# Kernel optimization log

Hardware: AMD Instinct MI355X
Metric: run time of the kernel (lower is better)

## Reference

```python
import jax, jax.numpy as jnp
import numpy as np

DIM = 16
BOND = 4
RANK = 512
N = 50000
E = 400000
F_IN = 16
EDGE_VARIABLE = 2


def setup_inputs() -> dict:
    key = jax.random.key(0)
    ks = iter(jax.random.split(key, 48))
    g = lambda shape, s=0.1: jax.random.normal(next(ks), shape, jnp.float32) * s
    inp = {
        "x": jax.random.normal(next(ks), (N, F_IN), jnp.float32),
        "node_type": jax.random.randint(next(ks), (N,), 0, 3),
        "edge_index": jax.random.randint(next(ks), (2, E), 0, N),
        "edge_attr": jax.random.uniform(next(ks), (E, BOND), dtype=jnp.float32),
        # lin0
        "W_lin0": g((F_IN, DIM)), "b_lin0": jnp.zeros((DIM,), jnp.float32),
        # NNConv: root weight + edge-conditioned weight MLP (4 -> 32 -> dim*dim)
        "W_root": g((DIM, DIM)), "b_conv": jnp.zeros((DIM,), jnp.float32),
        "W_e1": g((BOND, 32)), "b_e1": jnp.zeros((32,), jnp.float32),
        "W_e2": g((32, DIM * DIM)), "b_e2": jnp.zeros((DIM * DIM,), jnp.float32),
        # GRU (torch gate order r,z,n), weights stored torch-style [3*dim, dim]
        "W_ih": g((3 * DIM, DIM)), "b_ih": jnp.zeros((3 * DIM,), jnp.float32),
        "W_hh": g((3 * DIM, DIM)), "b_hh": jnp.zeros((3 * DIM,), jnp.float32),
        # projections
        "W_lin1": g((DIM, BOND)), "b_lin1": jnp.zeros((BOND,), jnp.float32),
        "W_up": g((BOND, DIM)), "b_up": jnp.zeros((DIM,), jnp.float32),
        "W_down": g((DIM, BOND)), "b_down": jnp.zeros((BOND,), jnp.float32),
        # FGNet low-rank factor modules (rank 512)
        "U_B": g((DIM, RANK)), "V_B": g((RANK, DIM)),
        "U_C": g((DIM, RANK)), "V_C": g((RANK, DIM)),
        "U_A": g((BOND, RANK)), "V_A": g((RANK, BOND)),
        # fusion weights
        "w_node": g((1, DIM)), "W_lin": g((DIM, DIM)), "b_lin": jnp.zeros((DIM,), jnp.float32),
        "w_edge": g((1, BOND)), "W_line": g((BOND, BOND)), "b_line": jnp.zeros((BOND,), jnp.float32),
    }
    return inp


def _forward(x, edge_attr, W_lin0, b_lin0, W_root, b_conv, W_e1, b_e1, W_e2, b_e2,
             W_ih, b_ih, W_hh, b_hh, W_lin1, b_lin1, W_up, b_up, W_down, b_down,
             U_B, V_B, U_C, V_C, U_A, V_A, w_node, W_lin, b_lin, w_edge, W_line, b_line,
             node_type, edge_index):
    src, dst = edge_index[0], edge_index[1]

    def nnconv(out):
        # per-edge weight matrices from edge features (edge-conditioned conv)
        he = jax.nn.relu(edge_attr @ W_e1 + b_e1)
        We = (he @ W_e2 + b_e2).reshape(E, DIM, DIM)          # [E, dim, dim]
        m = jnp.einsum('ed,edk->ek', out[src], We)             # gather-multiply
        agg = jax.ops.segment_sum(m, dst, num_segments=N)      # scatter-add
        deg = jax.ops.segment_sum(jnp.ones((E,), out.dtype), dst, num_segments=N)
        agg = agg / jnp.clip(deg, 1.0)[:, None]                # mean aggregation
        return out @ W_root + b_conv + agg

    def gru(inp, h):
        gi = inp @ W_ih.T + b_ih
        gh = h @ W_hh.T + b_hh
        i_r, i_z, i_n = jnp.split(gi, 3, axis=-1)
        h_r, h_z, h_n = jnp.split(gh, 3, axis=-1)
        r = jax.nn.sigmoid(i_r + h_r)
        z = jax.nn.sigmoid(i_z + h_z)
        n = jnp.tanh(i_n + r * h_n)
        return (1.0 - z) * n + z * h

    out = jax.nn.relu(x @ W_lin0 + b_lin0)                     # [N, dim]
    h = out
    for _ in range(3):
        m = jax.nn.relu(nnconv(out))
        h = gru(m, h)
        out = h

    out_edges = jax.nn.relu(out @ W_lin1 + b_lin1)             # [N, bond]

    # one outer message-passing round (k in range(1))
    ev_mask = (node_type == EDGE_VARIABLE)[:, None]
    out_edges_up = out_edges @ W_up + b_up                     # [N, dim]
    out_combine = jnp.where(ev_mask, out_edges_up, out)        # masked replace

    # factor-B message (low-rank FGNet) -> node-dim message + down-projected edge msg
    msg_B = jax.nn.relu((out_combine @ U_B) @ V_B)             # [N, dim]
    msg_to_edge_B = msg_B @ W_down + b_down                    # [N, bond]

    # factor-C message (low-rank FGNet)
    msg_C = jax.nn.relu((out_combine @ U_C) @ V_C)             # [N, dim]

    # factor-A / valence message on edge-type beliefs
    msg_to_edge_A = jax.nn.relu((out_edges @ U_A) @ V_A)       # [N, bond]

    all_msg = msg_B + msg_C                                    # sum over stacked msgs
    combine_edge_msg = msg_to_edge_A * msg_to_edge_B

    out = out + jax.nn.relu((w_node * all_msg) @ W_lin + b_lin)
    out_edges = out_edges + jax.nn.relu((w_edge * combine_edge_msg) @ W_line + b_line)

    return jax.nn.log_softmax(out_edges, axis=-1)              # [N, bond]


def reference(x, node_type, edge_index, edge_attr, W_lin0, b_lin0, W_root, b_conv,
              W_e1, b_e1, W_e2, b_e2, W_ih, b_ih, W_hh, b_hh, W_lin1, b_lin1,
              W_up, b_up, W_down, b_down, U_B, V_B, U_C, V_C, U_A, V_A,
              w_node, W_lin, b_lin, w_edge, W_line, b_line):
    return _forward(x, edge_attr, W_lin0, b_lin0, W_root, b_conv, W_e1, b_e1, W_e2, b_e2,
                    W_ih, b_ih, W_hh, b_hh, W_lin1, b_lin1, W_up, b_up, W_down, b_down,
                    U_B, V_B, U_C, V_C, U_A, V_A, w_node, W_lin, b_lin, w_edge, W_line, b_line,
                    node_type, edge_index)
```

## Files before the change

kernel.cpp:

```cpp
#include <hip/hip_runtime.h>
#include <hip/hip_bf16.h>
#include <math.h>

#define N_NODES 50000
#define N_EDGES 400000
#define DIM 16
#define BOND 4
#define NCHUNK 25000
#define EDGE_GRID 784
#define E_BLOCKS 1563
#define PRE_BASE (E_BLOCKS - 68)
#define SCAN_TILE 1024
#define SCAN_BLOCKS 49

typedef __attribute__((ext_vector_type(8))) short short8;
typedef __attribute__((ext_vector_type(4))) float f32x4;

__device__ __forceinline__ float bf16_to_f32(unsigned short v) {
  return __uint_as_float(((unsigned int)v) << 16);
}

__global__ __launch_bounds__(256) void setup_kernel(
    const float* __restrict__ x, const float* __restrict__ W_lin0,
    const float* __restrict__ b_lin0, const float* __restrict__ ea,
    const float* __restrict__ We1, const float* __restrict__ be1,
    const int* __restrict__ ei, const float* __restrict__ U_B,
    const float* __restrict__ V_B, const float* __restrict__ U_A,
    const float* __restrict__ V_A, float* __restrict__ out,
    unsigned int* __restrict__ he_buf, int* __restrict__ degI,
    float* __restrict__ M_B, float* __restrict__ M_A) {
  __shared__ float sW0[256];
  __shared__ float sb0[16];
  __shared__ float sW1[128];
  __shared__ float sb1[32];
  int t = threadIdx.x;
  sW0[t] = W_lin0[t];
  if (t < 16) sb0[t] = b_lin0[t];
  if (t < 128) sW1[t] = We1[t];
  if (t < 32) sb1[t] = be1[t];
  __syncthreads();

  int gid = blockIdx.x * 256 + t;

  if (gid < N_NODES) {
    float xr[16];
#pragma unroll
    for (int d = 0; d < 16; ++d) xr[d] = x[gid * 16 + d];
#pragma unroll
    for (int k = 0; k < 16; ++k) {
      float acc = sb0[k];
#pragma unroll
      for (int d = 0; d < 16; ++d) acc += xr[d] * sW0[d * 16 + k];
      out[gid * 16 + k] = fmaxf(acc, 0.f);
    }
  }

  if (gid < N_EDGES) {
    float4 v = ((const float4*)ea)[gid];
    float h[32];
#pragma unroll
    for (int k = 0; k < 32; ++k) {
      float a = sb1[k] + v.x * sW1[k] + v.y * sW1[32 + k] + v.z * sW1[64 + k] +
                v.w * sW1[96 + k];
      h[k] = fmaxf(a, 0.f);
    }
    unsigned int u[16];
#pragma unroll
    for (int p = 0; p < 2; ++p)
#pragma unroll
      for (int tt = 0; tt < 8; ++tt) {
        float2 pr;
        pr.x = h[4 * tt + p];
        pr.y = h[4 * tt + 2 + p];
        __hip_bfloat162 b = __float22bfloat162_rn(pr);
        u[p * 8 + tt] = *(unsigned int*)&b;
      }
    uint4* dst = (uint4*)(he_buf + (size_t)gid * 16);
#pragma unroll
    for (int qq = 0; qq < 4; ++qq)
      dst[qq] =
          make_uint4(u[4 * qq], u[4 * qq + 1], u[4 * qq + 2], u[4 * qq + 3]);
    atomicAdd(&degI[ei[N_EDGES + gid]], 1);
  }

  if (blockIdx.x >= PRE_BASE) {
    int w = (blockIdx.x - PRE_BASE) * 4 + (t >> 6);
    int lane = t & 63;
    float partial = 0.f;
    if (w < 256) {
      int i = w >> 4, j = w & 15;
#pragma unroll
      for (int r8 = 0; r8 < 8; ++r8) {
        int r = lane + 64 * r8;
        partial += U_B[i * 512 + r] * V_B[r * 16 + j];
      }
    } else if (w < 272) {
      int a = (w - 256) >> 2, b = (w - 256) & 3;
#pragma unroll
      for (int r8 = 0; r8 < 8; ++r8) {
        int r = lane + 64 * r8;
        partial += U_A[a * 512 + r] * V_A[r * 4 + b];
      }
    }
#pragma unroll
    for (int off = 32; off > 0; off >>= 1)
      partial += __shfl_down(partial, off);
    if (lane == 0) {
      if (w < 256) M_B[w] = partial;
      else if (w < 272) M_A[w - 256] = partial;
    }
  }
}

__global__ __launch_bounds__(256) void scan_kernel(
    const int* __restrict__ degI, int* ticket, int* st,
    int* __restrict__ row_off, int* __restrict__ cur) {
  __shared__ int sdata[256];
  __shared__ int s_tile;
  __shared__ int s_base;
  int t = threadIdx.x;
  if (t == 0) s_tile = atomicAdd(ticket, 1);
  __syncthreads();
  int tile = s_tile;
  int n0 = tile * SCAN_TILE + t * 4;

  int d0 = (n0 + 0 < N_NODES) ? degI[n0 + 0] : 0;
  int d1 = (n0 + 1 < N_NODES) ? degI[n0 + 1] : 0;
  int d2 = (n0 + 2 < N_NODES) ? degI[n0 + 2] : 0;
  int d3 = (n0 + 3 < N_NODES) ? degI[n0 + 3] : 0;
  int tsum = d0 + d1 + d2 + d3;
  sdata[t] = tsum;
  __syncthreads();
  for (int off = 1; off < 256; off <<= 1) {
    int v = (t >= off) ? sdata[t - off] : 0;
    __syncthreads();
    sdata[t] += v;
    __syncthreads();
  }
  int excl = sdata[t] - tsum;
  int agg = sdata[255];

  if (t == 0) {
    if (tile == 0) {
      atomicExch(&st[0], (agg << 2) | 2);
      s_base = 0;
    } else {
      atomicExch(&st[tile], (agg << 2) | 1);
      int run = 0, idx = tile - 1;
      while (true) {
        int w = atomicAdd(&st[idx], 0);
        int stt = w & 3;
        if (stt == 2) { run += (w >> 2); break; }
        if (stt == 1) { run += (w >> 2); --idx; }
      }
      atomicExch(&st[tile], ((run + agg) << 2) | 2);
      s_base = run;
    }
  }
  __syncthreads();

  int pre = s_base + excl;
  if (n0 + 0 < N_NODES) { row_off[n0 + 0] = pre; cur[n0 + 0] = pre; }
  pre += d0;
  if (n0 + 1 < N_NODES) { row_off[n0 + 1] = pre; cur[n0 + 1] = pre; }
  pre += d1;
  if (n0 + 2 < N_NODES) { row_off[n0 + 2] = pre; cur[n0 + 2] = pre; }
  pre += d2;
  if (n0 + 3 < N_NODES) { row_off[n0 + 3] = pre; cur[n0 + 3] = pre; }
  if (tile == SCAN_BLOCKS - 1 && t == 0) row_off[N_NODES] = N_EDGES;
}

__global__ __launch_bounds__(256) void slot_kernel(const int* __restrict__ ei,
                                                   int* __restrict__ cur,
                                                   int* __restrict__ slot) {
  int e = blockIdx.x * 256 + threadIdx.x;
  if (e < N_EDGES) slot[e] = atomicAdd(&cur[ei[N_EDGES + e]], 1);
}

__global__ __launch_bounds__(256) void edge_msg_mfma_kernel(
    const int* __restrict__ ei, const unsigned int* __restrict__ he_buf,
    const float* __restrict__ We2, const float* __restrict__ be2,
    const float* __restrict__ out, const int* __restrict__ slot,
    unsigned short* __restrict__ m_bufh) {
  const int lane = threadIdx.x & 63;
  const int q = lane >> 4, n = lane & 15;
  const int p = q >> 1, dbase = (q & 1) * 8;

  short8 bfrag[17];
#pragma unroll
  for (int s = 0; s < 16; ++s) {
    int h = 2 * s + p;
    union { short8 v; __hip_bfloat162 b2[4]; } bf;
#pragma unroll
    for (int jj = 0; jj < 4; ++jj) {
      float2 w;
      w.x = We2[h * 256 + (dbase + 2 * jj) * 16 + n];
      w.y = We2[h * 256 + (dbase + 2 * jj + 1) * 16 + n];
      bf.b2[jj] = __float22bfloat162_rn(w);
    }
    bfrag[s] = bf.v;
  }
  {
    union { short8 v; __hip_bfloat162 b2[4]; } bf;
#pragma unroll
    for (int jj = 0; jj < 4; ++jj) {
      float2 w;
      if (q < 2) {
        w.x = be2[(dbase + 2 * jj) * 16 + n];
        w.y = be2[(dbase + 2 * jj + 1) * 16 + n];
      } else {
        w.x = 0.f; w.y = 0.f;
      }
      bf.b2[jj] = __float22bfloat162_rn(w);
    }
    bfrag[16] = bf.v;
  }

  int wave = blockIdx.x * 4 + (threadIdx.x >> 6);
  const int nw = EDGE_GRID * 4;
  for (int c = wave; c < NCHUNK; c += nw) {
    int e = c * 16 + n;
    int src = ei[e];
    const uint4* hp = (const uint4*)(he_buf + (size_t)e * 16 + p * 8);
    uint4 h0 = hp[0], h1 = hp[1];
    unsigned int heu[8] = {h0.x, h0.y, h0.z, h0.w, h1.x, h1.y, h1.z, h1.w};
    const float4* op = (const float4*)(out + src * 16 + dbase);
    float4 o0 = op[0], o1 = op[1];
    float o[8] = {o0.x, o0.y, o0.z, o0.w, o1.x, o1.y, o1.z, o1.w};

    f32x4 acc = {0.f, 0.f, 0.f, 0.f};
#pragma unroll
    for (int s = 0; s < 16; ++s) {
      unsigned int hw = heu[s >> 1];
      float he_s = __uint_as_float((s & 1) ? (hw & 0xffff0000u) : (hw << 16));
      union { short8 v; __hip_bfloat162 b2[4]; } af;
#pragma unroll
      for (int jj = 0; jj < 4; ++jj) {
        float2 pr;
        pr.x = he_s * o[2 * jj];
        pr.y = he_s * o[2 * jj + 1];
        af.b2[jj] = __float22bfloat162_rn(pr);
      }
      acc = __builtin_amdgcn_mfma_f32_16x16x32_bf16(af.v, bfrag[s], acc, 0, 0, 0);
    }
    {
      union { short8 v; __hip_bfloat162 b2[4]; } af;
#pragma unroll
      for (int jj = 0; jj < 4; ++jj) {
        float2 pr;
        if (q < 2) { pr.x = o[2 * jj]; pr.y = o[2 * jj + 1]; }
        else { pr.x = 0.f; pr.y = 0.f; }
        af.b2[jj] = __float22bfloat162_rn(pr);
      }
      acc = __builtin_amdgcn_mfma_f32_16x16x32_bf16(af.v, bfrag[16], acc, 0, 0, 0);
    }

    int4 sl4 = *(const int4*)(slot + c * 16 + q * 4);
    __hip_bfloat16 b0 = __float2bfloat16(acc[0]);
    __hip_bfloat16 b1 = __float2bfloat16(acc[1]);
    __hip_bfloat16 b2 = __float2bfloat16(acc[2]);
    __hip_bfloat16 b3 = __float2bfloat16(acc[3]);
    m_bufh[(size_t)sl4.x * 16 + n] = *(unsigned short*)&b0;
    m_bufh[(size_t)sl4.y * 16 + n] = *(unsigned short*)&b1;
    m_bufh[(size_t)sl4.z * 16 + n] = *(unsigned short*)&b2;
    m_bufh[(size_t)sl4.w * 16 + n] = *(unsigned short*)&b3;
  }
}

__global__ __launch_bounds__(256) void gather_gru_kernel(
    const int* __restrict__ row_off, const unsigned short* __restrict__ m_bufh,
    const float* __restrict__ Wroot, const float* __restrict__ bconv,
    const float* __restrict__ Wih, const float* __restrict__ bih,
    const float* __restrict__ Whh, const float* __restrict__ bhh,
    float* __restrict__ out, int do_final, const int* __restrict__ node_type,
    const float* __restrict__ Wlin1, const float* __restrict__ blin1,
    const float* __restrict__ Wup, const float* __restrict__ bup,
    const float* __restrict__ Wdown, const float* __restrict__ bdown,
    const float* __restrict__ M_B, const float* __restrict__ M_A,
    const float* __restrict__ wedge, const float* __restrict__ Wline,
    const float* __restrict__ bline, float* __restrict__ res) {
  __shared__ float sWr[256];
  __shared__ float sWihT[768];
  __shared__ float sWhhT[768];
  __shared__ float sb[112];
  int t = threadIdx.x;
  int kk = t >> 4, dd = t & 15;
  sWr[t] = Wroot[t];
#pragma unroll
  for (int g = 0; g < 3; ++g) {
    sWihT[g * 256 + dd * 16 + kk] = Wih[g * 256 + t];
    sWhhT[g * 256 + dd * 16 + kk] = Whh[g * 256 + t];
  }
  if (t < 16) sb[t] = bconv[t];
  else if (t < 64) sb[t] = bih[t - 16];
  else if (t < 112) sb[t] = bhh[t - 64];
  __syncthreads();

  int n = blockIdx.x * 16 + (t >> 4);
  int k = t & 15;
  int s0 = row_off[n], s1 = row_off[n + 1];

  float aggk = 0.f;
  for (int j = s0; j < s1; ++j) aggk += bf16_to_f32(m_bufh[(size_t)j * 16 + k]);
  float sc = 1.f / fmaxf((float)(s1 - s0), 1.f);

  float hk = out[n * 16 + k];

  float mk = sb[k] + aggk * sc;
#pragma unroll
  for (int d = 0; d < 16; ++d) mk += __shfl(hk, d, 16) * sWr[d * 16 + k];
  mk = fmaxf(mk, 0.f);

  float gir = sb[16 + k], giz = sb[32 + k], gin = sb[48 + k];
  float ghr = sb[64 + k], ghz = sb[80 + k], ghn = sb[96 + k];
#pragma unroll
  for (int d = 0; d < 16; ++d) {
    float md = __shfl(mk, d, 16);
    float hd = __shfl(hk, d, 16);
    gir += md * sWihT[d * 16 + k];
    giz += md * sWihT[256 + d * 16 + k];
    gin += md * sWihT[512 + d * 16 + k];
    ghr += hd * sWhhT[d * 16 + k];
    ghz += hd * sWhhT[256 + d * 16 + k];
    ghn += hd * sWhhT[512 + d * 16 + k];
  }
  float r = 1.f / (1.f + __expf(-(gir + ghr)));
  float z = 1.f / (1.f + __expf(-(giz + ghz)));
  float xn = gin + r * ghn;
  float ng = 1.f - 2.f / (__expf(2.f * xn) + 1.f);
  float hnew = (1.f - z) * ng + z * hk;

  if (!do_final) {
    out[n * 16 + k] = hnew;
    return;
  }

  float p0 = hnew * Wlin1[k * 4 + 0];
  float p1 = hnew * Wlin1[k * 4 + 1];
  float p2 = hnew * Wlin1[k * 4 + 2];
  float p3 = hnew * Wlin1[k * 4 + 3];
#pragma unroll
  for (int msk = 1; msk < 16; msk <<= 1) {
    p0 += __shfl_xor(p0, msk, 16);
    p1 += __shfl_xor(p1, msk, 16);
    p2 += __shfl_xor(p2, msk, 16);
    p3 += __shfl_xor(p3, msk, 16);
  }
  float oe0 = fmaxf(p0 + blin1[0], 0.f);
  float oe1 = fmaxf(p1 + blin1[1], 0.f);
  float oe2 = fmaxf(p2 + blin1[2], 0.f);
  float oe3 = fmaxf(p3 + blin1[3], 0.f);

  bool ev = (node_type[n] == 2);
  float ock = ev ? (bup[k] + oe0 * Wup[k] + oe1 * Wup[16 + k] +
                    oe2 * Wup[32 + k] + oe3 * Wup[48 + k])
                 : hnew;

  float msgBk = 0.f;
#pragma unroll
  for (int d = 0; d < 16; ++d) msgBk += __shfl(ock, d, 16) * M_B[d * 16 + k];
  msgBk = fmaxf(msgBk, 0.f);

  float q0 = msgBk * Wdown[k * 4 + 0];
  float q1 = msgBk * Wdown[k * 4 + 1];
  float q2 = msgBk * Wdown[k * 4 + 2];
  float q3 = msgBk * Wdown[k * 4 + 3];
#pragma unroll
  for (int msk = 1; msk < 16; msk <<= 1) {
    q0 += __shfl_xor(q0, msk, 16);
    q1 += __shfl_xor(q1, msk, 16);
    q2 += __shfl_xor(q2, msk, 16);
    q3 += __shfl_xor(q3, msk, 16);
  }
  float mtb0 = q0 + bdown[0], mtb1 = q1 + bdown[1];
  float mtb2 = q2 + bdown[2], mtb3 = q3 + bdown[3];

  float mta0 = fmaxf(oe0 * M_A[0] + oe1 * M_A[4] + oe2 * M_A[8] + oe3 * M_A[12], 0.f);
  float mta1 = fmaxf(oe0 * M_A[1] + oe1 * M_A[5] + oe2 * M_A[9] + oe3 * M_A[13], 0.f);
  float mta2 = fmaxf(oe0 * M_A[2] + oe1 * M_A[6] + oe2 * M_A[10] + oe3 * M_A[14], 0.f);
  float mta3 = fmaxf(oe0 * M_A[3] + oe1 * M_A[7] + oe2 * M_A[11] + oe3 * M_A[15], 0.f);

  float c0 = wedge[0] * (mta0 * mtb0);
  float c1 = wedge[1] * (mta1 * mtb1);
  float c2 = wedge[2] * (mta2 * mtb2);
  float c3 = wedge[3] * (mta3 * mtb3);

  float f0 = oe0 + fmaxf(bline[0] + c0 * Wline[0] + c1 * Wline[4] +
                         c2 * Wline[8] + c3 * Wline[12], 0.f);
  float f1 = oe1 + fmaxf(bline[1] + c0 * Wline[1] + c1 * Wline[5] +
                         c2 * Wline[9] + c3 * Wline[13], 0.f);
  float f2 = oe2 + fmaxf(bline[2] + c0 * Wline[2] + c1 * Wline[6] +
                         c2 * Wline[10] + c3 * Wline[14], 0.f);
  float f3 = oe3 + fmaxf(bline[3] + c0 * Wline[3] + c1 * Wline[7] +
                         c2 * Wline[11] + c3 * Wline[15], 0.f);

  float mx = fmaxf(fmaxf(f0, f1), fmaxf(f2, f3));
  float se = __expf(f0 - mx) + __expf(f1 - mx) + __expf(f2 - mx) +
             __expf(f3 - mx);
  float lse = mx + __logf(se);
  if (k < 4) {
    float v = (k == 0) ? f0 : (k == 1) ? f1 : (k == 2) ? f2 : f3;
    res[n * 4 + k] = v - lse;
  }
}

extern "C" void kernel_launch(void* const* d_in, const int* in_sizes, int n_in,
                              void* d_out, int out_size, void* d_ws,
                              size_t ws_size, hipStream_t stream) {
  const float* x       = (const float*)d_in[0];
  const int* node_type = (const int*)d_in[1];
  const int* ei        = (const int*)d_in[2];
  const float* ea      = (const float*)d_in[3];
  const float* W_lin0  = (const float*)d_in[4];
  const float* b_lin0  = (const float*)d_in[5];
  const float* W_root  = (const float*)d_in[6];
  const float* b_conv  = (const float*)d_in[7];
  const float* W_e1    = (const float*)d_in[8];
  const float* b_e1    = (const float*)d_in[9];
  const float* W_e2    = (const float*)d_in[10];
  const float* b_e2    = (const float*)d_in[11];
  const float* W_ih    = (const float*)d_in[12];
  const float* b_ih    = (const float*)d_in[13];
  const float* W_hh    = (const float*)d_in[14];
  const float* b_hh    = (const float*)d_in[15];
  const float* W_lin1  = (const float*)d_in[16];
  const float* b_lin1  = (const float*)d_in[17];
  const float* W_up    = (const float*)d_in[18];
  const float* b_up    = (const float*)d_in[19];
  const float* W_down  = (const float*)d_in[20];
  const float* b_down  = (const float*)d_in[21];
  const float* U_B     = (const float*)d_in[22];
  const float* V_B     = (const float*)d_in[23];
  const float* U_A     = (const float*)d_in[26];
  const float* V_A     = (const float*)d_in[27];
  const float* w_edge  = (const float*)d_in[31];
  const float* W_line  = (const float*)d_in[32];
  const float* b_line  = (const float*)d_in[33];

  float* ws    = (float*)d_ws;
  float* out   = ws;
  unsigned int* he_buf = (unsigned int*)(out + N_NODES * 16);
  unsigned short* m_bufh =
      (unsigned short*)(he_buf + (size_t)N_EDGES * 16);
  float* M_B   = (float*)(m_bufh + (size_t)N_EDGES * 16);
  float* M_A   = M_B + 256;
  int* degI    = (int*)(M_A + 16);
  int* ticket  = degI + N_NODES;
  int* st      = ticket + 1;
  int* row_off = st + 63;
  int* cur     = row_off + N_NODES + 1;
  int* slot    = cur + N_NODES;

  hipMemsetAsync(degI, 0, (N_NODES + 64) * sizeof(int), stream);

  setup_kernel<<<E_BLOCKS, 256, 0, stream>>>(
      x, W_lin0, b_lin0, ea, W_e1, b_e1, ei, U_B, V_B, U_A, V_A, out, he_buf,
      degI, M_B, M_A);
  scan_kernel<<<SCAN_BLOCKS, 256, 0, stream>>>(degI, ticket, st, row_off, cur);
  slot_kernel<<<E_BLOCKS, 256, 0, stream>>>(ei, cur, slot);

  for (int it = 0; it < 3; ++it) {
    edge_msg_mfma_kernel<<<EDGE_GRID, 256, 0, stream>>>(ei, he_buf, W_e2, b_e2,
                                                        out, slot, m_bufh);
    gather_gru_kernel<<<N_NODES / 16, 256, 0, stream>>>(
        row_off, m_bufh, W_root, b_conv, W_ih, b_ih, W_hh, b_hh, out,
        (it == 2) ? 1 : 0, node_type, W_lin1, b_lin1, W_up, b_up, W_down,
        b_down, M_B, M_A, w_edge, W_line, b_line, (float*)d_out);
  }
}
```

Before: 344.8 us.

## Pre-sort edge hidden features and sources by destination to make message writes contiguous

Edge MLP first-layer features and source indices are now computed in the slot kernel and written directly in destination-sorted (CSR) order. The per-iteration edge kernel then reads sorted data and writes messages contiguously, replacing scattered per-slot stores and the slot array. The edge kernel grid is also enlarged to one block per chunk group. In exchange, the he buffer write in setup becomes a scattered write, done once, and source-node gathers in the edge kernel follow sorted order, which is no better localized.

```diff
diff --git a/kernel.cpp b/kernel.cpp
--- a/kernel.cpp
+++ b/kernel.cpp
@@ -4,14 +4,12 @@
 
 #define N_NODES 50000
 #define N_EDGES 400000
-#define DIM 16
-#define BOND 4
 #define NCHUNK 25000
-#define EDGE_GRID 784
 #define E_BLOCKS 1563
 #define PRE_BASE (E_BLOCKS - 68)
 #define SCAN_TILE 1024
 #define SCAN_BLOCKS 49
+#define EDGE_GRID 1563
 
 typedef __attribute__((ext_vector_type(8))) short short8;
 typedef __attribute__((ext_vector_type(4))) float f32x4;
@@ -22,22 +20,16 @@
 
 __global__ __launch_bounds__(256) void setup_kernel(
     const float* __restrict__ x, const float* __restrict__ W_lin0,
-    const float* __restrict__ b_lin0, const float* __restrict__ ea,
-    const float* __restrict__ We1, const float* __restrict__ be1,
-    const int* __restrict__ ei, const float* __restrict__ U_B,
-    const float* __restrict__ V_B, const float* __restrict__ U_A,
-    const float* __restrict__ V_A, float* __restrict__ out,
-    unsigned int* __restrict__ he_buf, int* __restrict__ degI,
-    float* __restrict__ M_B, float* __restrict__ M_A) {
+    const float* __restrict__ b_lin0, const int* __restrict__ ei,
+    const float* __restrict__ U_B, const float* __restrict__ V_B,
+    const float* __restrict__ U_A, const float* __restrict__ V_A,
+    float* __restrict__ out, int* __restrict__ degI, float* __restrict__ M_B,
+    float* __restrict__ M_A) {
   __shared__ float sW0[256];
   __shared__ float sb0[16];
-  __shared__ float sW1[128];
-  __shared__ float sb1[32];
   int t = threadIdx.x;
   sW0[t] = W_lin0[t];
   if (t < 16) sb0[t] = b_lin0[t];
-  if (t < 128) sW1[t] = We1[t];
-  if (t < 32) sb1[t] = be1[t];
   __syncthreads();
 
   int gid = blockIdx.x * 256 + t;
@@ -55,33 +47,7 @@
     }
   }
 
-  if (gid < N_EDGES) {
-    float4 v = ((const float4*)ea)[gid];
-    float h[32];
-#pragma unroll
-    for (int k = 0; k < 32; ++k) {
-      float a = sb1[k] + v.x * sW1[k] + v.y * sW1[32 + k] + v.z * sW1[64 + k] +
-                v.w * sW1[96 + k];
-      h[k] = fmaxf(a, 0.f);
-    }
-    unsigned int u[16];
-#pragma unroll
-    for (int p = 0; p < 2; ++p)
-#pragma unroll
-      for (int tt = 0; tt < 8; ++tt) {
-        float2 pr;
-        pr.x = h[4 * tt + p];
-        pr.y = h[4 * tt + 2 + p];
-        __hip_bfloat162 b = __float22bfloat162_rn(pr);
-        u[p * 8 + tt] = *(unsigned int*)&b;
-      }
-    uint4* dst = (uint4*)(he_buf + (size_t)gid * 16);
-#pragma unroll
-    for (int qq = 0; qq < 4; ++qq)
-      dst[qq] =
-          make_uint4(u[4 * qq], u[4 * qq + 1], u[4 * qq + 2], u[4 * qq + 3]);
-    atomicAdd(&degI[ei[N_EDGES + gid]], 1);
-  }
+  if (gid < N_EDGES) atomicAdd(&degI[ei[N_EDGES + gid]], 1);
 
   if (blockIdx.x >= PRE_BASE) {
     int w = (blockIdx.x - PRE_BASE) * 4 + (t >> 6);
@@ -103,8 +69,7 @@
       }
     }
 #pragma unroll
-    for (int off = 32; off > 0; off >>= 1)
-      partial += __shfl_down(partial, off);
+    for (int off = 32; off > 0; off >>= 1) partial += __shfl_down(partial, off);
     if (lane == 0) {
       if (w < 256) M_B[w] = partial;
       else if (w < 272) M_A[w - 256] = partial;
@@ -170,20 +135,55 @@
   if (tile == SCAN_BLOCKS - 1 && t == 0) row_off[N_NODES] = N_EDGES;
 }
 
-__global__ __launch_bounds__(256) void slot_kernel(const int* __restrict__ ei,
-                                                   int* __restrict__ cur,
-                                                   int* __restrict__ slot) {
-  int e = blockIdx.x * 256 + threadIdx.x;
-  if (e < N_EDGES) slot[e] = atomicAdd(&cur[ei[N_EDGES + e]], 1);
-}
-
-__global__ __launch_bounds__(256) void edge_msg_mfma_kernel(
-    const int* __restrict__ ei, const unsigned int* __restrict__ he_buf,
-    const float* __restrict__ We2, const float* __restrict__ be2,
-    const float* __restrict__ out, const int* __restrict__ slot,
+__global__ __launch_bounds__(256) void slot_kernel(
+    const int* __restrict__ ei, const float* __restrict__ ea,
+    const float* __restrict__ We1, const float* __restrict__ be1,
+    int* __restrict__ cur, int* __restrict__ src_sorted,
+    unsigned int* __restrict__ he_sorted) {
+  __shared__ float sW[128];
+  __shared__ float sb[32];
+  int t = threadIdx.x;
+  if (t < 128) sW[t] = We1[t];
+  if (t < 32) sb[t] = be1[t];
+  __syncthreads();
+  int e = blockIdx.x * 256 + t;
+  if (e >= N_EDGES) return;
+  int dst = ei[N_EDGES + e];
+  int s = atomicAdd(&cur[dst], 1);
+  src_sorted[s] = ei[e];
+
+  float4 v = ((const float4*)ea)[e];
+  float h[32];
+#pragma unroll
+  for (int k = 0; k < 32; ++k) {
+    float a = sb[k] + v.x * sW[k] + v.y * sW[32 + k] + v.z * sW[64 + k] +
+              v.w * sW[96 + k];
+    h[k] = fmaxf(a, 0.f);
+  }
+  unsigned int u[16];
+#pragma unroll
+  for (int p = 0; p < 2; ++p)
+#pragma unroll
+    for (int tt = 0; tt < 8; ++tt) {
+      float2 pr;
+      pr.x = h[4 * tt + p];
+      pr.y = h[4 * tt + 2 + p];
+      __hip_bfloat162 b = __float22bfloat162_rn(pr);
+      u[p * 8 + tt] = *(unsigned int*)&b;
+    }
+  uint4* dstp = (uint4*)(he_sorted + (size_t)s * 16);
+#pragma unroll
+  for (int qq = 0; qq < 4; ++qq)
+    dstp[qq] = make_uint4(u[4 * qq], u[4 * qq + 1], u[4 * qq + 2], u[4 * qq + 3]);
+}
+
+__global__ __launch_bounds__(256) void edge_kernel(
+    const int* __restrict__ src_sorted,
+    const unsigned int* __restrict__ he_sorted, const float* __restrict__ We2,
+    const float* __restrict__ be2, const float* __restrict__ out,
     unsigned short* __restrict__ m_bufh) {
   const int lane = threadIdx.x & 63;
-  const int q = lane >> 4, n = lane & 15;
+  const int q = lane >> 4, nn = lane & 15;
   const int p = q >> 1, dbase = (q & 1) * 8;
 
   short8 bfrag[17];
@@ -194,8 +194,8 @@
 #pragma unroll
     for (int jj = 0; jj < 4; ++jj) {
       float2 w;
-      w.x = We2[h * 256 + (dbase + 2 * jj) * 16 + n];
-      w.y = We2[h * 256 + (dbase + 2 * jj + 1) * 16 + n];
+      w.x = We2[h * 256 + (dbase + 2 * jj) * 16 + nn];
+      w.y = We2[h * 256 + (dbase + 2 * jj + 1) * 16 + nn];
       bf.b2[jj] = __float22bfloat162_rn(w);
     }
     bfrag[s] = bf.v;
@@ -206,8 +206,8 @@
     for (int jj = 0; jj < 4; ++jj) {
       float2 w;
       if (q < 2) {
-        w.x = be2[(dbase + 2 * jj) * 16 + n];
-        w.y = be2[(dbase + 2 * jj + 1) * 16 + n];
+        w.x = be2[(dbase + 2 * jj) * 16 + nn];
+        w.y = be2[(dbase + 2 * jj + 1) * 16 + nn];
       } else {
         w.x = 0.f; w.y = 0.f;
       }
@@ -219,9 +219,9 @@
   int wave = blockIdx.x * 4 + (threadIdx.x >> 6);
   const int nw = EDGE_GRID * 4;
   for (int c = wave; c < NCHUNK; c += nw) {
-    int e = c * 16 + n;
-    int src = ei[e];
-    const uint4* hp = (const uint4*)(he_buf + (size_t)e * 16 + p * 8);
+    int e = c * 16 + nn;
+    int src = src_sorted[e];
+    const uint4* hp = (const uint4*)(he_sorted + (size_t)e * 16 + p * 8);
     uint4 h0 = hp[0], h1 = hp[1];
     unsigned int heu[8] = {h0.x, h0.y, h0.z, h0.w, h1.x, h1.y, h1.z, h1.w};
     const float4* op = (const float4*)(out + src * 16 + dbase);
@@ -255,15 +255,11 @@
       acc = __builtin_amdgcn_mfma_f32_16x16x32_bf16(af.v, bfrag[16], acc, 0, 0, 0);
     }
 
-    int4 sl4 = *(const int4*)(slot + c * 16 + q * 4);
-    __hip_bfloat16 b0 = __float2bfloat16(acc[0]);
-    __hip_bfloat16 b1 = __float2bfloat16(acc[1]);
-    __hip_bfloat16 b2 = __float2bfloat16(acc[2]);
-    __hip_bfloat16 b3 = __float2bfloat16(acc[3]);
-    m_bufh[(size_t)sl4.x * 16 + n] = *(unsigned short*)&b0;
-    m_bufh[(size_t)sl4.y * 16 + n] = *(unsigned short*)&b1;
-    m_bufh[(size_t)sl4.z * 16 + n] = *(unsigned short*)&b2;
-    m_bufh[(size_t)sl4.w * 16 + n] = *(unsigned short*)&b3;
+#pragma unroll
+    for (int r = 0; r < 4; ++r) {
+      __hip_bfloat16 w = __float2bfloat16(acc[r]);
+      m_bufh[(size_t)(c * 16 + q * 4 + r) * 16 + nn] = *(unsigned short*)&w;
+    }
   }
 }
 
@@ -385,14 +381,10 @@
   float c2 = wedge[2] * (mta2 * mtb2);
   float c3 = wedge[3] * (mta3 * mtb3);
 
-  float f0 = oe0 + fmaxf(bline[0] + c0 * Wline[0] + c1 * Wline[4] +
-                         c2 * Wline[8] + c3 * Wline[12], 0.f);
-  float f1 = oe1 + fmaxf(bline[1] + c0 * Wline[1] + c1 * Wline[5] +
-                         c2 * Wline[9] + c3 * Wline[13], 0.f);
-  float f2 = oe2 + fmaxf(bline[2] + c0 * Wline[2] + c1 * Wline[6] +
-                         c2 * Wline[10] + c3 * Wline[14], 0.f);
-  float f3 = oe3 + fmaxf(bline[3] + c0 * Wline[3] + c1 * Wline[7] +
-                         c2 * Wline[11] + c3 * Wline[15], 0.f);
+  float f0 = oe0 + fmaxf(bline[0] + c0 * Wline[0] + c1 * Wline[4] + c2 * Wline[8] + c3 * Wline[12], 0.f);
+  float f1 = oe1 + fmaxf(bline[1] + c0 * Wline[1] + c1 * Wline[5] + c2 * Wline[9] + c3 * Wline[13], 0.f);
+  float f2 = oe2 + fmaxf(bline[2] + c0 * Wline[2] + c1 * Wline[6] + c2 * Wline[10] + c3 * Wline[14], 0.f);
+  float f3 = oe3 + fmaxf(bline[3] + c0 * Wline[3] + c1 * Wline[7] + c2 * Wline[11] + c3 * Wline[15], 0.f);
 
   float mx = fmaxf(fmaxf(f0, f1), fmaxf(f2, f3));
   float se = __expf(f0 - mx) + __expf(f1 - mx) + __expf(f2 - mx) +
@@ -437,31 +429,31 @@
   const float* W_line  = (const float*)d_in[32];
   const float* b_line  = (const float*)d_in[33];
 
-  float* ws    = (float*)d_ws;
-  float* out   = ws;
-  unsigned int* he_buf = (unsigned int*)(out + N_NODES * 16);
+  float* ws = (float*)d_ws;
+  float* out = ws;
+  unsigned int* he_sorted = (unsigned int*)(out + N_NODES * 16);
   unsigned short* m_bufh =
-      (unsigned short*)(he_buf + (size_t)N_EDGES * 16);
-  float* M_B   = (float*)(m_bufh + (size_t)N_EDGES * 16);
-  float* M_A   = M_B + 256;
-  int* degI    = (int*)(M_A + 16);
-  int* ticket  = degI + N_NODES;
-  int* st      = ticket + 1;
-  int* row_off = st + 63;
-  int* cur     = row_off + N_NODES + 1;
-  int* slot    = cur + N_NODES;
+      (unsigned short*)(he_sorted + (size_t)N_EDGES * 16);
+  int* src_sorted = (int*)(m_bufh + (size_t)N_EDGES * 16);
+  float* M_B = (float*)(src_sorted + N_EDGES);
+  float* M_A = M_B + 256;
+  int* row_off = (int*)(M_A + 16);
+  int* cur = row_off + N_NODES + 4;
+  int* degI = cur + N_NODES;
+  int* ticket = degI + N_NODES;
+  int* st = ticket + 1;
 
   hipMemsetAsync(degI, 0, (N_NODES + 64) * sizeof(int), stream);
 
-  setup_kernel<<<E_BLOCKS, 256, 0, stream>>>(
-      x, W_lin0, b_lin0, ea, W_e1, b_e1, ei, U_B, V_B, U_A, V_A, out, he_buf,
-      degI, M_B, M_A);
+  setup_kernel<<<E_BLOCKS, 256, 0, stream>>>(x, W_lin0, b_lin0, ei, U_B, V_B,
+                                             U_A, V_A, out, degI, M_B, M_A);
   scan_kernel<<<SCAN_BLOCKS, 256, 0, stream>>>(degI, ticket, st, row_off, cur);
-  slot_kernel<<<E_BLOCKS, 256, 0, stream>>>(ei, cur, slot);
+  slot_kernel<<<E_BLOCKS, 256, 0, stream>>>(ei, ea, W_e1, b_e1, cur, src_sorted,
+                                            he_sorted);
 
   for (int it = 0; it < 3; ++it) {
-    edge_msg_mfma_kernel<<<EDGE_GRID, 256, 0, stream>>>(ei, he_buf, W_e2, b_e2,
-                                                        out, slot, m_bufh);
+    edge_kernel<<<EDGE_GRID, 256, 0, stream>>>(src_sorted, he_sorted, W_e2,
+                                               b_e2, out, m_bufh);
     gather_gru_kernel<<<N_NODES / 16, 256, 0, stream>>>(
         row_off, m_bufh, W_root, b_conv, W_ih, b_ih, W_hh, b_hh, out,
         (it == 2) ? 1 : 0, node_type, W_lin1, b_lin1, W_up, b_up, W_down,
```

New measurement: 350.4 us. About the same (+1.6%).
